# Kernel tuning notes

Hardware: AMD Instinct MI355X
Metric: run time of the kernel (lower is better)

The kernel has to match this reference:

```python
import jax, jax.numpy as jnp
import numpy as np

B = 8          # batch
RES = 64       # resolution (H = W)
DIM = 512      # channels
HEADS = 8
HD = DIM // HEADS   # 64
HSP, WSP = RES, 8   # idx=0: H_sp=resolution, W_sp=split_size
NH, NW = RES // HSP, RES // WSP   # windows per axis


def setup_inputs() -> dict:
    key = jax.random.key(0)
    k1, k2, k3 = jax.random.split(key, 3)
    qkv = jax.random.normal(k1, (3, B, RES * RES, DIM), dtype=jnp.float32)
    lepe_w = jax.random.normal(k2, (DIM, 1, 3, 3), dtype=jnp.float32) * 0.1
    lepe_b = jax.random.normal(k3, (DIM,), dtype=jnp.float32) * 0.1
    return {"qkv": qkv, "lepe_w": lepe_w, "lepe_b": lepe_b}


def _to_windows(t):
    # [B, L, C] row-major -> [B*NH*NW, HSP*WSP, C]; equivalent to the
    # block-diagonal flex_attention mask grouping (y//H_sp, x//W_sp).
    t = t.reshape(B, NH, HSP, NW, WSP, DIM)
    return t.transpose(0, 1, 3, 2, 4, 5).reshape(B * NH * NW, HSP * WSP, DIM)


def _from_windows(t):
    t = t.reshape(B, NH, NW, HSP, WSP, DIM).transpose(0, 1, 3, 2, 4, 5)
    return t.reshape(B, RES * RES, DIM)


def reference(qkv, lepe_w, lepe_b):
    q, k, v = qkv[0], qkv[1], qkv[2]            # each [B, L, C]
    qw, kw, vw = _to_windows(q), _to_windows(k), _to_windows(v)

    # LePE: depthwise 3x3 conv on v laid out per-window as [n, C, HSP, WSP]
    vimg = vw.transpose(0, 2, 1).reshape(-1, DIM, HSP, WSP)
    lepe = jax.lax.conv_general_dilated(
        vimg, lepe_w, window_strides=(1, 1), padding='SAME',
        dimension_numbers=('NCHW', 'OIHW', 'NCHW'), feature_group_count=DIM)
    lepe = lepe + lepe_b[None, :, None, None]
    lepe = lepe.reshape(-1, DIM, HSP * WSP).transpose(0, 2, 1)  # [n, T, C]

    def split_heads(t):
        return t.reshape(t.shape[0], t.shape[1], HEADS, HD)

    qh, kh, vh, lh = map(split_heads, (qw, kw, vw, lepe))
    scale = 1.0 / np.sqrt(HD).astype(np.float32)  # flex_attention default scale
    scores = jnp.einsum('wqhd,wkhd->whqk', qh, kh) * scale
    attn = jax.nn.softmax(scores, axis=-1)
    out = jnp.einsum('whqk,wkhd->wqhd', attn, vh) + lh   # [n, T, H, hd]
    out = out.reshape(out.shape[0], out.shape[1], DIM)
    return _from_windows(out)
```

## Files before the change

kernel.cpp:

```cpp
#include <hip/hip_runtime.h>
#include <hip/hip_bf16.h>

#define RESV 64
#define DIMV 512
#define HDV 64
#define TWIN 512
#define KSTR 68
#define VSTR 516

typedef __bf16 bf16x8_t __attribute__((ext_vector_type(8)));
typedef float f32x4_t __attribute__((ext_vector_type(4)));

union Frag {
  bf16x8_t v;
  unsigned short u[8];
  unsigned int w[4];
};

__device__ __forceinline__ unsigned short f2bf(float f) {
  unsigned int u = __builtin_bit_cast(unsigned int, f);
  u += 0x7fffu + ((u >> 16) & 1u);
  return (unsigned short)(u >> 16);
}
__device__ __forceinline__ float bf2f(unsigned int h) {
  return __builtin_bit_cast(float, h << 16);
}

__global__ __launch_bounds__(512, 2)
void lepe_attn_kernel(const float* __restrict__ qkv,
                      const float* __restrict__ lw,
                      const float* __restrict__ lb,
                      float* __restrict__ out)
{
  __shared__ unsigned short K_lds[TWIN * KSTR];
  __shared__ unsigned short Vt_lds[HDV * VSTR];

  const int head = blockIdx.x & 7;
  const int win  = blockIdx.x >> 3;
  const int bat  = win >> 3;
  const int nw   = win & 7;

  const int tid  = threadIdx.x;
  const int wave = tid >> 6;
  const int lane = tid & 63;
  const int l15  = lane & 15;
  const int g    = lane >> 4;

  const float* qptr = qkv;
  const float* kptr = qkv + 16777216;
  const float* vptr = qkv + 2 * 16777216;

  const int rowbase = bat * 4096;

  {
    const int tK = wave * 64 + (lane >> 5);
    const int c2 = (lane & 31) * 2;
    #pragma unroll 4
    for (int i = 0; i < 32; ++i) {
      int t = tK + i * 2;
      int grow = rowbase + (t >> 3) * 64 + nw * 8 + (t & 7);
      const float2 f = *(const float2*)(kptr + (size_t)grow * DIMV + head * HDV + c2);
      unsigned int pk = (unsigned int)f2bf(f.x) | ((unsigned int)f2bf(f.y) << 16);
      *(unsigned int*)&K_lds[t * KSTR + c2] = pk;
    }
    #pragma unroll 4
    for (int i = 0; i < 64; ++i) {
      int t = wave * 64 + i;
      int grow = rowbase + (t >> 3) * 64 + nw * 8 + (t & 7);
      float v = vptr[(size_t)grow * DIMV + head * HDV + lane];
      Vt_lds[lane * VSTR + t] = f2bf(v);
    }
  }

  const int qbase = wave * 64;
  Frag qf[4][2];
  #pragma unroll
  for (int qi = 0; qi < 4; ++qi) {
    int tok = qbase + qi * 16 + l15;
    int grow = rowbase + (tok >> 3) * 64 + nw * 8 + (tok & 7);
    const float* qp = qptr + (size_t)grow * DIMV + head * HDV;
    #pragma unroll
    for (int kc = 0; kc < 2; ++kc) {
      const float4 f0 = *(const float4*)(qp + kc * 32 + 4 * g);
      const float4 f1 = *(const float4*)(qp + kc * 32 + 4 * g + 16);
      qf[qi][kc].u[0] = f2bf(f0.x); qf[qi][kc].u[1] = f2bf(f0.y);
      qf[qi][kc].u[2] = f2bf(f0.z); qf[qi][kc].u[3] = f2bf(f0.w);
      qf[qi][kc].u[4] = f2bf(f1.x); qf[qi][kc].u[5] = f2bf(f1.y);
      qf[qi][kc].u[6] = f2bf(f1.z); qf[qi][kc].u[7] = f2bf(f1.w);
    }
  }

  __syncthreads();

  const f32x4_t zero4 = {0.f, 0.f, 0.f, 0.f};
  f32x4_t ot[4][4];
  #pragma unroll
  for (int di = 0; di < 4; ++di)
    #pragma unroll
    for (int qi = 0; qi < 4; ++qi)
      ot[di][qi] = zero4;
  float lsum[4] = {0.f, 0.f, 0.f, 0.f};

  for (int kt = 0; kt < 8; ++kt) {
    f32x4_t st[4][4];
    #pragma unroll
    for (int ki = 0; ki < 4; ++ki)
      #pragma unroll
      for (int qi = 0; qi < 4; ++qi)
        st[ki][qi] = zero4;

    #pragma unroll
    for (int kc = 0; kc < 2; ++kc) {
      Frag kf[4];
      #pragma unroll
      for (int ki = 0; ki < 4; ++ki) {
        const unsigned short* kp = &K_lds[(kt * 64 + ki * 16 + l15) * KSTR + kc * 32 + 4 * g];
        *(uint2*)&kf[ki].w[0] = *(const uint2*)kp;
        *(uint2*)&kf[ki].w[2] = *(const uint2*)(kp + 16);
      }
      #pragma unroll
      for (int ki = 0; ki < 4; ++ki)
        #pragma unroll
        for (int qi = 0; qi < 4; ++qi)
          st[ki][qi] = __builtin_amdgcn_mfma_f32_16x16x32_bf16(
              kf[ki].v, qf[qi][kc].v, st[ki][qi], 0, 0, 0);
    }

    #pragma unroll
    for (int ki = 0; ki < 4; ++ki)
      #pragma unroll
      for (int qi = 0; qi < 4; ++qi) {
        f32x4_t s = st[ki][qi];
        #pragma unroll
        for (int r = 0; r < 4; ++r) {
          float p = __expf(s[r] * 0.125f);
          s[r] = p;
          lsum[qi] += p;
        }
        st[ki][qi] = s;
      }

    #pragma unroll
    for (int kb = 0; kb < 2; ++kb) {
      Frag vf[4];
      #pragma unroll
      for (int di = 0; di < 4; ++di) {
        const unsigned short* vp = &Vt_lds[(di * 16 + l15) * VSTR + kt * 64 + kb * 32 + 4 * g];
        *(uint2*)&vf[di].w[0] = *(const uint2*)vp;
        *(uint2*)&vf[di].w[2] = *(const uint2*)(vp + 16);
      }
      #pragma unroll
      for (int qi = 0; qi < 4; ++qi) {
        Frag pb;
        #pragma unroll
        for (int r = 0; r < 4; ++r) {
          pb.u[r]     = f2bf(st[2 * kb][qi][r]);
          pb.u[4 + r] = f2bf(st[2 * kb + 1][qi][r]);
        }
        #pragma unroll
        for (int di = 0; di < 4; ++di)
          ot[di][qi] = __builtin_amdgcn_mfma_f32_16x16x32_bf16(
              vf[di].v, pb.v, ot[di][qi], 0, 0, 0);
      }
    }
  }

  float rl[4];
  #pragma unroll
  for (int qi = 0; qi < 4; ++qi) {
    float s = lsum[qi];
    s += __shfl_xor(s, 16, 64);
    s += __shfl_xor(s, 32, 64);
    rl[qi] = 1.0f / s;
  }

  __syncthreads();

  unsigned short* lepe = &K_lds[wave * 64 * KSTR];
  {
    float wgt[9];
    const float* wp = lw + (size_t)(head * HDV + lane) * 9;
    #pragma unroll
    for (int tp = 0; tp < 9; ++tp) wgt[tp] = wp[tp];
    const float bias = lb[head * HDV + lane];
    const int y0 = wave * 8;

    float rm[8], rc[8], rp[8];
    auto loadrow = [&](int y, float* dst) {
      if (y < 0 || y > 63) {
        #pragma unroll
        for (int x = 0; x < 8; ++x) dst[x] = 0.f;
        return;
      }
      const unsigned short* p = &Vt_lds[lane * VSTR + y * 8];
      uint2 a = *(const uint2*)p;
      uint2 c = *(const uint2*)(p + 4);
      dst[0] = bf2f(a.x & 0xffffu); dst[1] = bf2f(a.x >> 16);
      dst[2] = bf2f(a.y & 0xffffu); dst[3] = bf2f(a.y >> 16);
      dst[4] = bf2f(c.x & 0xffffu); dst[5] = bf2f(c.x >> 16);
      dst[6] = bf2f(c.y & 0xffffu); dst[7] = bf2f(c.y >> 16);
    };
    loadrow(y0 - 1, rm);
    loadrow(y0, rc);
    for (int yy = 0; yy < 8; ++yy) {
      loadrow(y0 + yy + 1, rp);
      #pragma unroll
      for (int x = 0; x < 8; ++x) {
        float acc = bias;
        if (x > 0) acc += rm[x - 1] * wgt[0] + rc[x - 1] * wgt[3] + rp[x - 1] * wgt[6];
        acc += rm[x] * wgt[1] + rc[x] * wgt[4] + rp[x] * wgt[7];
        if (x < 7) acc += rm[x + 1] * wgt[2] + rc[x + 1] * wgt[5] + rp[x + 1] * wgt[8];
        lepe[(yy * 8 + x) * KSTR + lane] = f2bf(acc);
      }
      #pragma unroll
      for (int x = 0; x < 8; ++x) { rm[x] = rc[x]; rc[x] = rp[x]; }
    }
  }

  __syncthreads();

  #pragma unroll
  for (int qi = 0; qi < 4; ++qi) {
    int tloc = qi * 16 + l15;
    int tok = qbase + tloc;
    int grow = rowbase + (tok >> 3) * 64 + nw * 8 + (tok & 7);
    float* op = out + (size_t)grow * DIMV + head * HDV;
    #pragma unroll
    for (int di = 0; di < 4; ++di) {
      const unsigned short* lp = &lepe[tloc * KSTR + di * 16 + 4 * g];
      uint2 lv = *(const uint2*)lp;
      float4 o;
      o.x = ot[di][qi][0] * rl[qi] + bf2f(lv.x & 0xffffu);
      o.y = ot[di][qi][1] * rl[qi] + bf2f(lv.x >> 16);
      o.z = ot[di][qi][2] * rl[qi] + bf2f(lv.y & 0xffffu);
      o.w = ot[di][qi][3] * rl[qi] + bf2f(lv.y >> 16);
      *(float4*)(op + di * 16 + 4 * g) = o;
    }
  }
}

extern "C" void kernel_launch(void* const* d_in, const int* in_sizes, int n_in,
                              void* d_out, int out_size, void* d_ws, size_t ws_size,
                              hipStream_t stream) {
  const float* qkv = (const float*)d_in[0];
  const float* lw  = (const float*)d_in[1];
  const float* lb  = (const float*)d_in[2];
  float* out = (float*)d_out;
  (void)in_sizes; (void)n_in; (void)out_size; (void)d_ws; (void)ws_size;

  dim3 grid(512);
  dim3 block(512);
  hipLaunchKernelGGL(lepe_attn_kernel, grid, block, 0, stream, qkv, lw, lb, out);
}
```

Before: 91.26 us.

## Stream K/V tiles through double-buffered swizzled LDS with 16 waves per block

Replaces full-window K/V staging in LDS with a loop that streams 64-token K/V tiles through double-buffered, XOR-swizzled LDS, prefetching the next tile from global memory while computing the current one. The block grows to 1024 threads, each wave owning 32 queries, and LDS use drops so more blocks can be resident. The LePE convolution now reads V directly from global memory in fp32 and is fused into the output epilogue. This trades a large upfront load and LDS footprint for more barriers per tile and redundant global reads of V for the convolution.

```diff
diff --git a/kernel.cpp b/kernel.cpp
--- a/kernel.cpp
+++ b/kernel.cpp
@@ -1,12 +1,8 @@
 #include <hip/hip_runtime.h>
 #include <hip/hip_bf16.h>
 
-#define RESV 64
 #define DIMV 512
 #define HDV 64
-#define TWIN 512
-#define KSTR 68
-#define VSTR 516
 
 typedef __bf16 bf16x8_t __attribute__((ext_vector_type(8)));
 typedef float f32x4_t __attribute__((ext_vector_type(4)));
@@ -15,25 +11,28 @@
   bf16x8_t v;
   unsigned short u[8];
   unsigned int w[4];
+  uint2 d[2];
 };
 
 __device__ __forceinline__ unsigned short f2bf(float f) {
-  unsigned int u = __builtin_bit_cast(unsigned int, f);
-  u += 0x7fffu + ((u >> 16) & 1u);
-  return (unsigned short)(u >> 16);
+  return __builtin_bit_cast(unsigned short, (__bf16)f);
 }
 __device__ __forceinline__ float bf2f(unsigned int h) {
   return __builtin_bit_cast(float, h << 16);
 }
 
-__global__ __launch_bounds__(512, 2)
+#define KTILE_B 8192
+#define VTILE_B 9216
+#define VBASE   16384
+#define SMEM_B  34816
+
+__global__ __launch_bounds__(1024, 4)
 void lepe_attn_kernel(const float* __restrict__ qkv,
                       const float* __restrict__ lw,
                       const float* __restrict__ lb,
                       float* __restrict__ out)
 {
-  __shared__ unsigned short K_lds[TWIN * KSTR];
-  __shared__ unsigned short Vt_lds[HDV * VSTR];
+  __shared__ __align__(16) unsigned char smem[SMEM_B];
 
   const int head = blockIdx.x & 7;
   const int win  = blockIdx.x >> 3;
@@ -48,41 +47,47 @@
 
   const float* qptr = qkv;
   const float* kptr = qkv + 16777216;
-  const float* vptr = qkv + 2 * 16777216;
-
+  const float* vptr = qkv + 33554432;
   const int rowbase = bat * 4096;
 
-  {
-    const int tK = wave * 64 + (lane >> 5);
-    const int c2 = (lane & 31) * 2;
-    #pragma unroll 4
-    for (int i = 0; i < 32; ++i) {
-      int t = tK + i * 2;
-      int grow = rowbase + (t >> 3) * 64 + nw * 8 + (t & 7);
-      const float2 f = *(const float2*)(kptr + (size_t)grow * DIMV + head * HDV + c2);
-      unsigned int pk = (unsigned int)f2bf(f.x) | ((unsigned int)f2bf(f.y) << 16);
-      *(unsigned int*)&K_lds[t * KSTR + c2] = pk;
-    }
-    #pragma unroll 4
-    for (int i = 0; i < 64; ++i) {
-      int t = wave * 64 + i;
-      int grow = rowbase + (t >> 3) * 64 + nw * 8 + (t & 7);
-      float v = vptr[(size_t)grow * DIMV + head * HDV + lane];
-      Vt_lds[lane * VSTR + t] = f2bf(v);
-    }
-  }
-
-  const int qbase = wave * 64;
-  Frag qf[4][2];
-  #pragma unroll
-  for (int qi = 0; qi < 4; ++qi) {
-    int tok = qbase + qi * 16 + l15;
-    int grow = rowbase + (tok >> 3) * 64 + nw * 8 + (tok & 7);
-    const float* qp = qptr + (size_t)grow * DIMV + head * HDV;
+  auto growf = [&](int tok) -> size_t {
+    return ((size_t)(rowbase + ((tok >> 3) << 6) + (nw << 3) + (tok & 7))) * DIMV
+           + head * HDV;
+  };
+
+  const int st_t = (wave << 2) + g;
+  const int st_c = l15;
+  const float* kg = kptr + growf(st_t) + 4 * st_c;
+  const float* vg = vptr + growf(st_t) + 4 * st_c;
+
+  const int ksw = (st_t & 7) << 4;
+  const int kwb = st_t * 128 + ((st_c * 8) ^ ksw);
+  const int vwb = (st_c * 4) * 144 + 2 * st_t;
+
+  auto stage_write = [&](int buf, const float4& kv, const float4& vv) {
+    unsigned char* kb = smem + buf * KTILE_B;
+    uint2 kp;
+    kp.x = (unsigned)f2bf(kv.x) | ((unsigned)f2bf(kv.y) << 16);
+    kp.y = (unsigned)f2bf(kv.z) | ((unsigned)f2bf(kv.w) << 16);
+    *(uint2*)(kb + kwb) = kp;
+    unsigned char* vb = smem + VBASE + buf * VTILE_B;
+    *(unsigned short*)(vb + vwb)       = f2bf(vv.x);
+    *(unsigned short*)(vb + vwb + 144) = f2bf(vv.y);
+    *(unsigned short*)(vb + vwb + 288) = f2bf(vv.z);
+    *(unsigned short*)(vb + vwb + 432) = f2bf(vv.w);
+  };
+
+  float4 kin = *(const float4*)kg;
+  float4 vin = *(const float4*)vg;
+
+  Frag qf[2][2];
+  #pragma unroll
+  for (int qi = 0; qi < 2; ++qi) {
+    const float* qp = qptr + growf(wave * 32 + qi * 16 + l15);
     #pragma unroll
     for (int kc = 0; kc < 2; ++kc) {
-      const float4 f0 = *(const float4*)(qp + kc * 32 + 4 * g);
-      const float4 f1 = *(const float4*)(qp + kc * 32 + 4 * g + 16);
+      float4 f0 = *(const float4*)(qp + kc * 32 + 4 * g);
+      float4 f1 = *(const float4*)(qp + kc * 32 + 4 * g + 16);
       qf[qi][kc].u[0] = f2bf(f0.x); qf[qi][kc].u[1] = f2bf(f0.y);
       qf[qi][kc].u[2] = f2bf(f0.z); qf[qi][kc].u[3] = f2bf(f0.w);
       qf[qi][kc].u[4] = f2bf(f1.x); qf[qi][kc].u[5] = f2bf(f1.y);
@@ -90,72 +95,85 @@
     }
   }
 
+  stage_write(0, kin, vin);
   __syncthreads();
 
   const f32x4_t zero4 = {0.f, 0.f, 0.f, 0.f};
-  f32x4_t ot[4][4];
+  f32x4_t ot[4][2];
   #pragma unroll
   for (int di = 0; di < 4; ++di)
     #pragma unroll
-    for (int qi = 0; qi < 4; ++qi)
-      ot[di][qi] = zero4;
-  float lsum[4] = {0.f, 0.f, 0.f, 0.f};
-
+    for (int qi = 0; qi < 2; ++qi) ot[di][qi] = zero4;
+  float lsum[2] = {0.f, 0.f};
+
+  #pragma unroll 2
   for (int kt = 0; kt < 8; ++kt) {
-    f32x4_t st[4][4];
-    #pragma unroll
-    for (int ki = 0; ki < 4; ++ki)
-      #pragma unroll
-      for (int qi = 0; qi < 4; ++qi)
-        st[ki][qi] = zero4;
-
-    #pragma unroll
-    for (int kc = 0; kc < 2; ++kc) {
-      Frag kf[4];
-      #pragma unroll
-      for (int ki = 0; ki < 4; ++ki) {
-        const unsigned short* kp = &K_lds[(kt * 64 + ki * 16 + l15) * KSTR + kc * 32 + 4 * g];
-        *(uint2*)&kf[ki].w[0] = *(const uint2*)kp;
-        *(uint2*)&kf[ki].w[2] = *(const uint2*)(kp + 16);
-      }
-      #pragma unroll
-      for (int ki = 0; ki < 4; ++ki)
-        #pragma unroll
-        for (int qi = 0; qi < 4; ++qi)
-          st[ki][qi] = __builtin_amdgcn_mfma_f32_16x16x32_bf16(
-              kf[ki].v, qf[qi][kc].v, st[ki][qi], 0, 0, 0);
-    }
-
-    #pragma unroll
-    for (int ki = 0; ki < 4; ++ki)
-      #pragma unroll
-      for (int qi = 0; qi < 4; ++qi) {
-        f32x4_t s = st[ki][qi];
+    if (kt < 7) {
+      kin = *(const float4*)(kg + (size_t)(kt + 1) * 262144);
+      vin = *(const float4*)(vg + (size_t)(kt + 1) * 262144);
+    }
+    const unsigned char* kb = smem + (kt & 1) * KTILE_B;
+    const unsigned char* vb = smem + VBASE + (kt & 1) * VTILE_B;
+
+    #pragma unroll
+    for (int hb = 0; hb < 2; ++hb) {
+      Frag kf[2][2];
+      #pragma unroll
+      for (int kc = 0; kc < 2; ++kc)
+        #pragma unroll
+        for (int ki = 0; ki < 2; ++ki) {
+          int row = hb * 32 + ki * 16 + l15;
+          int sw = (row & 7) << 4;
+          int cb = kc * 64 + 8 * g;
+          const unsigned char* p = kb + row * 128;
+          kf[kc][ki].d[0] = *(const uint2*)(p + (cb ^ sw));
+          kf[kc][ki].d[1] = *(const uint2*)(p + ((cb + 32) ^ sw));
+        }
+
+      f32x4_t st[2][2];
+      #pragma unroll
+      for (int ki = 0; ki < 2; ++ki)
+        #pragma unroll
+        for (int qi = 0; qi < 2; ++qi) st[ki][qi] = zero4;
+
+      #pragma unroll
+      for (int kc = 0; kc < 2; ++kc)
+        #pragma unroll
+        for (int ki = 0; ki < 2; ++ki)
+          #pragma unroll
+          for (int qi = 0; qi < 2; ++qi)
+            st[ki][qi] = __builtin_amdgcn_mfma_f32_16x16x32_bf16(
+                kf[kc][ki].v, qf[qi][kc].v, st[ki][qi], 0, 0, 0);
+
+      #pragma unroll
+      for (int ki = 0; ki < 2; ++ki)
+        #pragma unroll
+        for (int qi = 0; qi < 2; ++qi) {
+          f32x4_t s = st[ki][qi];
+          #pragma unroll
+          for (int r = 0; r < 4; ++r) {
+            float p = __expf(s[r] * 0.125f);
+            s[r] = p;
+            lsum[qi] += p;
+          }
+          st[ki][qi] = s;
+        }
+
+      Frag vf[4];
+      #pragma unroll
+      for (int di = 0; di < 4; ++di) {
+        int byte = (di * 16 + l15) * 144 + hb * 64 + 8 * g;
+        vf[di].d[0] = *(const uint2*)(vb + byte);
+        vf[di].d[1] = *(const uint2*)(vb + byte + 32);
+      }
+
+      #pragma unroll
+      for (int qi = 0; qi < 2; ++qi) {
+        Frag pb;
         #pragma unroll
         for (int r = 0; r < 4; ++r) {
-          float p = __expf(s[r] * 0.125f);
-          s[r] = p;
-          lsum[qi] += p;
-        }
-        st[ki][qi] = s;
-      }
-
-    #pragma unroll
-    for (int kb = 0; kb < 2; ++kb) {
-      Frag vf[4];
-      #pragma unroll
-      for (int di = 0; di < 4; ++di) {
-        const unsigned short* vp = &Vt_lds[(di * 16 + l15) * VSTR + kt * 64 + kb * 32 + 4 * g];
-        *(uint2*)&vf[di].w[0] = *(const uint2*)vp;
-        *(uint2*)&vf[di].w[2] = *(const uint2*)(vp + 16);
-      }
-      #pragma unroll
-      for (int qi = 0; qi < 4; ++qi) {
-        Frag pb;
-        #pragma unroll
-        for (int r = 0; r < 4; ++r) {
-          pb.u[r]     = f2bf(st[2 * kb][qi][r]);
-          pb.u[4 + r] = f2bf(st[2 * kb + 1][qi][r]);
+          pb.u[r]     = f2bf(st[0][qi][r]);
+          pb.u[4 + r] = f2bf(st[1][qi][r]);
         }
         #pragma unroll
         for (int di = 0; di < 4; ++di)
@@ -163,78 +181,83 @@
               vf[di].v, pb.v, ot[di][qi], 0, 0, 0);
       }
     }
-  }
-
-  float rl[4];
-  #pragma unroll
-  for (int qi = 0; qi < 4; ++qi) {
+
+    if (kt < 7) stage_write((kt + 1) & 1, kin, vin);
+    __syncthreads();
+  }
+
+  float rl[2];
+  #pragma unroll
+  for (int qi = 0; qi < 2; ++qi) {
     float s = lsum[qi];
     s += __shfl_xor(s, 16, 64);
     s += __shfl_xor(s, 32, 64);
     rl[qi] = 1.0f / s;
   }
 
-  __syncthreads();
-
-  unsigned short* lepe = &K_lds[wave * 64 * KSTR];
+  unsigned char* lep = smem + wave * 2176;
+  float wgt[9];
   {
-    float wgt[9];
     const float* wp = lw + (size_t)(head * HDV + lane) * 9;
     #pragma unroll
-    for (int tp = 0; tp < 9; ++tp) wgt[tp] = wp[tp];
-    const float bias = lb[head * HDV + lane];
-    const int y0 = wave * 8;
-
-    float rm[8], rc[8], rp[8];
-    auto loadrow = [&](int y, float* dst) {
-      if (y < 0 || y > 63) {
-        #pragma unroll
-        for (int x = 0; x < 8; ++x) dst[x] = 0.f;
-        return;
-      }
-      const unsigned short* p = &Vt_lds[lane * VSTR + y * 8];
-      uint2 a = *(const uint2*)p;
-      uint2 c = *(const uint2*)(p + 4);
-      dst[0] = bf2f(a.x & 0xffffu); dst[1] = bf2f(a.x >> 16);
-      dst[2] = bf2f(a.y & 0xffffu); dst[3] = bf2f(a.y >> 16);
-      dst[4] = bf2f(c.x & 0xffffu); dst[5] = bf2f(c.x >> 16);
-      dst[6] = bf2f(c.y & 0xffffu); dst[7] = bf2f(c.y >> 16);
-    };
-    loadrow(y0 - 1, rm);
-    loadrow(y0, rc);
-    for (int yy = 0; yy < 8; ++yy) {
-      loadrow(y0 + yy + 1, rp);
-      #pragma unroll
-      for (int x = 0; x < 8; ++x) {
-        float acc = bias;
-        if (x > 0) acc += rm[x - 1] * wgt[0] + rc[x - 1] * wgt[3] + rp[x - 1] * wgt[6];
-        acc += rm[x] * wgt[1] + rc[x] * wgt[4] + rp[x] * wgt[7];
-        if (x < 7) acc += rm[x + 1] * wgt[2] + rc[x + 1] * wgt[5] + rp[x + 1] * wgt[8];
-        lepe[(yy * 8 + x) * KSTR + lane] = f2bf(acc);
-      }
-      #pragma unroll
-      for (int x = 0; x < 8; ++x) { rm[x] = rc[x]; rc[x] = rp[x]; }
-    }
-  }
-
-  __syncthreads();
-
-  #pragma unroll
-  for (int qi = 0; qi < 4; ++qi) {
-    int tloc = qi * 16 + l15;
-    int tok = qbase + tloc;
-    int grow = rowbase + (tok >> 3) * 64 + nw * 8 + (tok & 7);
-    float* op = out + (size_t)grow * DIMV + head * HDV;
+    for (int i = 0; i < 9; ++i) wgt[i] = wp[i];
+  }
+  const float bias = lb[head * HDV + lane];
+  const int yb = wave * 4;
+
+  float ra[8], rb2[8], rc2[8], rd[8];
+  auto loadrow = [&](int y, float* dst) {
+    if ((unsigned)y < 64u) {
+      const float* p = vptr + ((size_t)(rowbase + y * 64 + nw * 8)) * DIMV
+                       + head * HDV + lane;
+      #pragma unroll
+      for (int x = 0; x < 8; ++x) dst[x] = p[(size_t)x * DIMV];
+    } else {
+      #pragma unroll
+      for (int x = 0; x < 8; ++x) dst[x] = 0.f;
+    }
+  };
+  loadrow(yb - 1, ra);
+  loadrow(yb,     rb2);
+  loadrow(yb + 1, rc2);
+
+  #pragma unroll
+  for (int qi = 0; qi < 2; ++qi) {
+    loadrow(yb + 2 * qi + 2, rd);
+    #pragma unroll
+    for (int x = 0; x < 8; ++x) {
+      float a0 = bias, a1 = bias;
+      if (x > 0) {
+        a0 += ra[x-1]*wgt[0] + rb2[x-1]*wgt[3] + rc2[x-1]*wgt[6];
+        a1 += rb2[x-1]*wgt[0] + rc2[x-1]*wgt[3] + rd[x-1]*wgt[6];
+      }
+      a0 += ra[x]*wgt[1] + rb2[x]*wgt[4] + rc2[x]*wgt[7];
+      a1 += rb2[x]*wgt[1] + rc2[x]*wgt[4] + rd[x]*wgt[7];
+      if (x < 7) {
+        a0 += ra[x+1]*wgt[2] + rb2[x+1]*wgt[5] + rc2[x+1]*wgt[8];
+        a1 += rb2[x+1]*wgt[2] + rc2[x+1]*wgt[5] + rd[x+1]*wgt[8];
+      }
+      *(unsigned short*)(lep + x * 136 + 2 * lane)       = f2bf(a0);
+      *(unsigned short*)(lep + (8 + x) * 136 + 2 * lane) = f2bf(a1);
+    }
+
+    const float rlq = rl[qi];
+    float* op = out + growf(wave * 32 + qi * 16 + l15);
     #pragma unroll
     for (int di = 0; di < 4; ++di) {
-      const unsigned short* lp = &lepe[tloc * KSTR + di * 16 + 4 * g];
-      uint2 lv = *(const uint2*)lp;
+      uint2 lv = *(const uint2*)(lep + l15 * 136 + di * 32 + 8 * g);
       float4 o;
-      o.x = ot[di][qi][0] * rl[qi] + bf2f(lv.x & 0xffffu);
-      o.y = ot[di][qi][1] * rl[qi] + bf2f(lv.x >> 16);
-      o.z = ot[di][qi][2] * rl[qi] + bf2f(lv.y & 0xffffu);
-      o.w = ot[di][qi][3] * rl[qi] + bf2f(lv.y >> 16);
+      o.x = ot[di][qi][0] * rlq + bf2f(lv.x & 0xffffu);
+      o.y = ot[di][qi][1] * rlq + bf2f(lv.x >> 16);
+      o.z = ot[di][qi][2] * rlq + bf2f(lv.y & 0xffffu);
+      o.w = ot[di][qi][3] * rlq + bf2f(lv.y >> 16);
       *(float4*)(op + di * 16 + 4 * g) = o;
+    }
+
+    if (qi == 0) {
+      #pragma unroll
+      for (int x = 0; x < 8; ++x) { ra[x] = rc2[x]; rb2[x] = rd[x]; }
+      loadrow(yb + 3, rc2);
     }
   }
 }
@@ -249,6 +272,6 @@
   (void)in_sizes; (void)n_in; (void)out_size; (void)d_ws; (void)ws_size;
 
   dim3 grid(512);
-  dim3 block(512);
+  dim3 block(1024);
   hipLaunchKernelGGL(lepe_attn_kernel, grid, block, 0, stream, qkv, lw, lb, out);
 }
```

Result: slower. 155.7 us (+70.6%).
